# Kernel optimization log

Hardware: AMD Instinct MI355X
Metric: run time of the kernel (lower is better)

## Reference

```python
import jax, jax.numpy as jnp
import numpy as np

N_ENTITY = 100000
N_RELATION = 32
DIM = 64
N_LAYER = 2
B = 4096
T = 64


def setup_inputs() -> dict:
    key = jax.random.key(0)
    ks = jax.random.split(key, 12)
    inp = {
        "items": jax.random.randint(ks[0], (B,), 0, N_ENTITY),
        "user_h": jax.random.randint(ks[1], (N_LAYER, B, T), 0, N_ENTITY),
        "user_r": jax.random.randint(ks[2], (N_LAYER, B, T), 0, N_RELATION),
        "user_t": jax.random.randint(ks[3], (N_LAYER, B, T), 0, N_ENTITY),
        "item_h": jax.random.randint(ks[4], (N_LAYER, B, T), 0, N_ENTITY),
        "item_r": jax.random.randint(ks[5], (N_LAYER, B, T), 0, N_RELATION),
        "item_t": jax.random.randint(ks[6], (N_LAYER, B, T), 0, N_ENTITY),
        # parameters (xavier-ish scale)
        "entity_emb": jax.random.normal(ks[7], (N_ENTITY, DIM), jnp.float32) * 0.05,
        "relation_emb": jax.random.normal(ks[8], (N_RELATION, DIM), jnp.float32) * 0.05,
        # torch Linear(in,out,bias=False) stored here as [in, out] so y = x @ W
        "W1": jax.random.normal(ks[9], (2 * DIM, DIM), jnp.float32) * 0.1,
        "W2": jax.random.normal(ks[10], (DIM, DIM), jnp.float32) * 0.1,
        "W3": jax.random.normal(ks[11], (DIM, 1), jnp.float32) * 0.1,
    }
    return inp


def reference(items, user_h, user_r, user_t, item_h, item_r, item_t,
              entity_emb, relation_emb, W1, W2, W3):
    def knowledge_attention(h_idx, r_idx, t_idx):
        h = entity_emb[h_idx]        # [B, T, d]
        r = relation_emb[r_idx]      # [B, T, d]
        t = entity_emb[t_idx]        # [B, T, d]
        x = jnp.concatenate([h, r], axis=-1)           # [B, T, 2d]
        a = jax.nn.relu(x @ W1)                        # [B, T, d]
        a = jax.nn.relu(a @ W2)                        # [B, T, d]
        a = jax.nn.sigmoid(jnp.squeeze(a @ W3, -1))    # [B, T]
        w = jax.nn.softmax(a, axis=-1)                 # softmax over triples
        return jnp.sum(w[..., None] * t, axis=1)       # [B, d]

    # user embeddings: origin = mean of hop-0 heads, then attention per layer; agg='sum'
    e_u = jnp.mean(entity_emb[user_h[0]], axis=1)
    for i in range(N_LAYER):
        e_u = e_u + knowledge_attention(user_h[i], user_r[i], user_t[i])

    # item embeddings: origin = item entity emb, attention per layer,
    # plus (agg=='sum', n_layer>0) extra mean of hop-0 heads
    e_v = entity_emb[items]
    for i in range(N_LAYER):
        e_v = e_v + knowledge_attention(item_h[i], item_r[i], item_t[i])
    e_v = e_v + jnp.mean(entity_emb[item_h[0]], axis=1)

    scores = jax.nn.sigmoid(jnp.sum(e_v * e_u, axis=1))  # [B]
    return scores
```

## Files before the change

kernel.cpp:

```cpp
#include <hip/hip_runtime.h>
#include <hip/hip_bf16.h>
#include <cstdint>

#define DEV static __device__ __forceinline__

typedef float        v4f __attribute__((ext_vector_type(4)));
typedef float        v2f __attribute__((ext_vector_type(2)));
typedef short        v8s __attribute__((ext_vector_type(8)));
typedef unsigned int v4u __attribute__((ext_vector_type(4)));

static constexpr int N_ENT = 100000;
static constexpr int BATCH = 4096;

DEV unsigned short f2bf(float f) {
    __hip_bfloat16 h = __float2bfloat16(f);
    return __builtin_bit_cast(unsigned short, h);
}
DEV unsigned int pkbf(float lo, float hi) {
    return (unsigned)f2bf(lo) | ((unsigned)f2bf(hi) << 16);
}
DEV float bflo(unsigned int w) { return __uint_as_float(w << 16); }
DEV float bfhi(unsigned int w) { return __uint_as_float(w & 0xffff0000u); }
DEV v2f up2(unsigned int w) { return (v2f){bflo(w), bfhi(w)}; }

DEV void glds16(const void* g, void* l) {
    __builtin_amdgcn_global_load_lds(
        (const __attribute__((address_space(1))) unsigned int*)g,
        (__attribute__((address_space(3))) unsigned int*)l, 16, 0, 0);
}

__global__ void k0_prep(const float* __restrict__ rel, const float* __restrict__ W1,
                        const float* __restrict__ W2,
                        unsigned short* __restrict__ R1b, unsigned short* __restrict__ W2p,
                        unsigned short* __restrict__ W1p)
{
    const int gid = blockIdx.x * 256 + threadIdx.x;
    if (gid < 2048) {
        const int r = gid >> 6, j = gid & 63;
        float acc = 0.f;
        #pragma unroll 8
        for (int k = 0; k < 64; ++k)
            acc += rel[r * 64 + k] * W1[(64 + k) * 64 + j];
        R1b[gid] = f2bf(acc);
    } else if (gid < 2048 + 4096) {
        const int f = gid - 2048;
        const int i = f & 7, l = (f >> 3) & 63;
        const int tn = (f >> 9) & 3, kk = f >> 11;
        W2p[f] = f2bf(W2[(32 * kk + 8 * (l >> 4) + i) * 64 + 16 * tn + (l & 15)]);
    } else if (gid < 2048 + 8192) {
        const int f = gid - 6144;
        const int i = f & 7, l = (f >> 3) & 63;
        const int tn = (f >> 9) & 3, kk = f >> 11;
        W1p[f] = f2bf(W1[(32 * kk + 8 * (l >> 4) + i) * 64 + 16 * tn + (l & 15)]);
    }
}

__global__ void __launch_bounds__(256) k1_e1(const float* __restrict__ emb,
                                             const unsigned short* __restrict__ W1p,
                                             unsigned short* __restrict__ E1,
                                             unsigned short* __restrict__ E0)
{
    const int lane = threadIdx.x & 63;
    const int q = lane & 15, g = lane >> 4;
    const int wid = blockIdx.x * 4 + (threadIdx.x >> 6);
    const int e0 = wid * 16;
    if (e0 >= N_ENT) return;

    v8s af[2];
    #pragma unroll
    for (int kk = 0; kk < 2; ++kk) {
        const float* p = emb + (size_t)(e0 + q) * 64 + 32 * kk + 8 * g;
        const v4f x = *(const v4f*)p;
        const v4f y = *(const v4f*)(p + 4);
        v4u pk;
        pk[0] = pkbf(x[0], x[1]); pk[1] = pkbf(x[2], x[3]);
        pk[2] = pkbf(y[0], y[1]); pk[3] = pkbf(y[2], y[3]);
        af[kk] = __builtin_bit_cast(v8s, pk);
        *(v4u*)(E0 + (size_t)(e0 + q) * 64 + 32 * kk + 8 * g) = pk;
    }

    v4f acc[4];
    #pragma unroll
    for (int tn = 0; tn < 4; ++tn) acc[tn] = (v4f){0.f, 0.f, 0.f, 0.f};
    #pragma unroll
    for (int kk = 0; kk < 2; ++kk)
        #pragma unroll
        for (int tn = 0; tn < 4; ++tn) {
            const v8s bfr = *(const v8s*)(W1p + ((kk * 4 + tn) * 64 + lane) * 8);
            acc[tn] = __builtin_amdgcn_mfma_f32_16x16x32_bf16(af[kk], bfr, acc[tn], 0, 0, 0);
        }
    #pragma unroll
    for (int tn = 0; tn < 4; ++tn)
        #pragma unroll
        for (int i = 0; i < 4; ++i)
            E1[(size_t)(e0 + 4 * g + i) * 64 + 16 * tn + q] = f2bf(acc[tn][i]);
}

__global__ void __launch_bounds__(256) k2_fused(
    const int* __restrict__ items,
    const int* __restrict__ user_h, const int* __restrict__ user_r, const int* __restrict__ user_t,
    const int* __restrict__ item_h, const int* __restrict__ item_r, const int* __restrict__ item_t,
    const float* __restrict__ emb, const unsigned short* __restrict__ E0,
    const unsigned short* __restrict__ E1,
    const unsigned short* __restrict__ R1b, const unsigned short* __restrict__ W2p,
    const float* __restrict__ W3, float* __restrict__ out)
{
    __shared__ float ws_w[4][64];
    __shared__ float att_s[4][64];
    __shared__ float mp[4][64];
    __shared__ __align__(16) unsigned char e0s[4][8192];
    __shared__ __align__(16) unsigned char m0s[4][4096];

    const int lane  = threadIdx.x & 63;
    const int b     = blockIdx.x;
    const int combo = threadIdx.x >> 6;
    const int layer = combo & 1;
    const int side  = combo >> 1, half = combo & 1;
    const int* Hp; const int* Rp; const int* Tp;
    if (combo < 2) { Hp = user_h; Rp = user_r; Tp = user_t; }
    else           { Hp = item_h; Rp = item_r; Tp = item_t; }
    const int base = (layer * BATCH + b) * 64;
    const int* H0p = (side ? item_h : user_h) + b * 64;

    const int q = lane & 15, g = lane >> 4;
    const int sub = lane & 7, grp = lane >> 3;

    int hidx[4], ridx[4];
    #pragma unroll
    for (int tm = 0; tm < 4; ++tm) {
        hidx[tm] = Hp[base + 16 * tm + q];
        ridx[tm] = Rp[base + 16 * tm + q];
    }
    const int tv = Tp[base + lane];
    int midx[4];
    #pragma unroll
    for (int it = 0; it < 4; ++it) midx[it] = H0p[32 * half + 8 * it + grp];

    v4u ev[4][2], rv[4][2];
    #pragma unroll
    for (int tm = 0; tm < 4; ++tm)
        #pragma unroll
        for (int kk = 0; kk < 2; ++kk) {
            ev[tm][kk] = *(const v4u*)(E1  + (size_t)hidx[tm] * 64 + 32 * kk + 8 * g);
            rv[tm][kk] = *(const v4u*)(R1b + (size_t)ridx[tm] * 64 + 32 * kk + 8 * g);
        }

    #pragma unroll
    for (int it = 0; it < 8; ++it) {
        const int tr = __shfl(tv, 8 * it + grp);
        glds16(E0 + (size_t)tr * 64 + sub * 8, &e0s[combo][it * 1024]);
    }
    #pragma unroll
    for (int it = 0; it < 4; ++it)
        glds16(E0 + (size_t)midx[it] * 64 + sub * 8, &m0s[combo][it * 1024]);
    __builtin_amdgcn_sched_barrier(0);

    float w3v[4];
    #pragma unroll
    for (int tn = 0; tn < 4; ++tn) w3v[tn] = W3[16 * tn + q];

    float p[4][4];
    #pragma unroll
    for (int tm = 0; tm < 4; ++tm) {
        v4f a4[4];
        #pragma unroll
        for (int tn = 0; tn < 4; ++tn) a4[tn] = (v4f){0.f, 0.f, 0.f, 0.f};
        #pragma unroll
        for (int kk = 0; kk < 2; ++kk) {
            v4u afu;
            #pragma unroll
            for (int w = 0; w < 4; ++w) {
                const unsigned int e = ev[tm][kk][w], r = rv[tm][kk][w];
                afu[w] = pkbf(fmaxf(bflo(e) + bflo(r), 0.f),
                              fmaxf(bfhi(e) + bfhi(r), 0.f));
            }
            const v8s af = __builtin_bit_cast(v8s, afu);
            #pragma unroll
            for (int tn = 0; tn < 4; ++tn) {
                const v8s bfr = *(const v8s*)(W2p + ((kk * 4 + tn) * 64 + lane) * 8);
                a4[tn] = __builtin_amdgcn_mfma_f32_16x16x32_bf16(af, bfr, a4[tn], 0, 0, 0);
            }
        }
        #pragma unroll
        for (int i = 0; i < 4; ++i) {
            float s = 0.f;
            #pragma unroll
            for (int tn = 0; tn < 4; ++tn)
                s += fmaxf(a4[tn][i], 0.f) * w3v[tn];
            p[tm][i] = s;
        }
    }
    #pragma unroll
    for (int m = 1; m <= 8; m <<= 1)
        #pragma unroll
        for (int tm = 0; tm < 4; ++tm)
            #pragma unroll
            for (int i = 0; i < 4; ++i)
                p[tm][i] += __shfl_xor(p[tm][i], m);

    float ee[4][4];
    float sloc = 0.f;
    #pragma unroll
    for (int tm = 0; tm < 4; ++tm)
        #pragma unroll
        for (int i = 0; i < 4; ++i) {
            const float sg = 1.f / (1.f + __expf(-p[tm][i]));
            const float ex = __expf(sg);
            ee[tm][i] = ex;
            sloc += ex;
        }
    sloc += __shfl_xor(sloc, 16);
    sloc += __shfl_xor(sloc, 32);
    const float rS = 1.f / sloc;

    if (q == 0) {
        #pragma unroll
        for (int tm = 0; tm < 4; ++tm) {
            v4f wv;
            #pragma unroll
            for (int i = 0; i < 4; ++i) wv[i] = ee[tm][i] * rS;
            *(v4f*)&ws_w[combo][16 * tm + 4 * g] = wv;
        }
    }

    asm volatile("s_waitcnt vmcnt(0)" ::: "memory");
    __builtin_amdgcn_sched_barrier(0);

    v2f a2[4], m2[4];
    #pragma unroll
    for (int c = 0; c < 4; ++c) { a2[c] = (v2f){0.f, 0.f}; m2[c] = (v2f){0.f, 0.f}; }
    #pragma unroll
    for (int it = 0; it < 8; ++it) {
        const float w = ws_w[combo][8 * it + grp];
        const v2f wv = (v2f){w, w};
        const v4u e = *(const v4u*)&e0s[combo][it * 1024 + lane * 16];
        #pragma unroll
        for (int c = 0; c < 4; ++c) a2[c] += wv * up2(e[c]);
    }
    #pragma unroll
    for (int it = 0; it < 4; ++it) {
        const v4u e = *(const v4u*)&m0s[combo][it * 1024 + lane * 16];
        #pragma unroll
        for (int c = 0; c < 4; ++c) m2[c] += up2(e[c]);
    }
    #pragma unroll
    for (int m = 8; m <= 32; m <<= 1)
        #pragma unroll
        for (int c = 0; c < 4; ++c) {
            a2[c][0] += __shfl_xor(a2[c][0], m);
            a2[c][1] += __shfl_xor(a2[c][1], m);
            m2[c][0] += __shfl_xor(m2[c][0], m);
            m2[c][1] += __shfl_xor(m2[c][1], m);
        }
    if (lane < 8) {
        #pragma unroll
        for (int c = 0; c < 4; ++c) {
            att_s[combo][lane * 8 + 2 * c]     = a2[c][0];
            att_s[combo][lane * 8 + 2 * c + 1] = a2[c][1];
            mp[combo][lane * 8 + 2 * c]        = m2[c][0];
            mp[combo][lane * 8 + 2 * c + 1]    = m2[c][1];
        }
    }
    __syncthreads();

    if (threadIdx.x < 64) {
        const int j = lane;
        const float itemv = emb[(size_t)items[b] * 64 + j];
        const float eu = att_s[0][j] + att_s[1][j] + (mp[0][j] + mp[1][j]) * (1.f / 64.f);
        const float evv = itemv + att_s[2][j] + att_s[3][j]
                        + (mp[2][j] + mp[3][j]) * (1.f / 64.f);
        float d = eu * evv;
        #pragma unroll
        for (int m = 1; m <= 32; m <<= 1) d += __shfl_xor(d, m);
        if (lane == 0) out[b] = 1.f / (1.f + __expf(-d));
    }
}

extern "C" void kernel_launch(void* const* d_in, const int* in_sizes, int n_in,
                              void* d_out, int out_size, void* d_ws, size_t ws_size,
                              hipStream_t stream)
{
    const int*   items  = (const int*)d_in[0];
    const int*   user_h = (const int*)d_in[1];
    const int*   user_r = (const int*)d_in[2];
    const int*   user_t = (const int*)d_in[3];
    const int*   item_h = (const int*)d_in[4];
    const int*   item_r = (const int*)d_in[5];
    const int*   item_t = (const int*)d_in[6];
    const float* emb    = (const float*)d_in[7];
    const float* rel    = (const float*)d_in[8];
    const float* W1     = (const float*)d_in[9];
    const float* W2     = (const float*)d_in[10];
    const float* W3     = (const float*)d_in[11];
    float* out = (float*)d_out;

    char* ws = (char*)d_ws;
    const size_t tb = (size_t)N_ENT * 64 * 2;
    unsigned short* E0  = (unsigned short*)ws;
    unsigned short* E1  = (unsigned short*)(ws + tb);
    unsigned short* R1b = (unsigned short*)(ws + 2 * tb);
    unsigned short* W2p = (unsigned short*)(ws + 2 * tb + 4096);
    unsigned short* W1p = (unsigned short*)(ws + 2 * tb + 4096 + 8192);

    hipLaunchKernelGGL(k0_prep, dim3(40), dim3(256), 0, stream, rel, W1, W2, R1b, W2p, W1p);
    hipLaunchKernelGGL(k1_e1, dim3((6250 + 3) / 4), dim3(256), 0, stream, emb, W1p, E1, E0);
    hipLaunchKernelGGL(k2_fused, dim3(BATCH), dim3(256), 0, stream,
                       items, user_h, user_r, user_t, item_h, item_r, item_t,
                       emb, E0, E1, R1b, W2p, W3, out);
}
```

Measured before the change: 79.28 us.

## Split each attention combo across two waves with 512-thread blocks

The fused kernel now runs 8 waves per block instead of 4. Each (side, layer) combo is split across two waves that each handle 32 of the 64 triples. Softmax normalization moves to the end: each wave writes its partial denominator to shared memory and the final reduction divides by the combined sums. W2 fragments are preloaded into registers, and index loads are coalesced and redistributed with shuffles. The aim is more memory-level parallelism and shorter per-wave latency chains, at the cost of more waves per block and extra shared-memory bookkeeping.

```diff
diff --git a/kernel.cpp b/kernel.cpp
--- a/kernel.cpp
+++ b/kernel.cpp
@@ -96,7 +96,7 @@
             E1[(size_t)(e0 + 4 * g + i) * 64 + 16 * tn + q] = f2bf(acc[tn][i]);
 }
 
-__global__ void __launch_bounds__(256) k2_fused(
+__global__ void __launch_bounds__(512) k2_fused(
     const int* __restrict__ items,
     const int* __restrict__ user_h, const int* __restrict__ user_r, const int* __restrict__ user_t,
     const int* __restrict__ item_h, const int* __restrict__ item_r, const int* __restrict__ item_t,
@@ -106,62 +106,75 @@
     const float* __restrict__ W3, float* __restrict__ out)
 {
     __shared__ float ws_w[4][64];
-    __shared__ float att_s[4][64];
-    __shared__ float mp[4][64];
-    __shared__ __align__(16) unsigned char e0s[4][8192];
-    __shared__ __align__(16) unsigned char m0s[4][4096];
+    __shared__ float att_s[8][64];
+    __shared__ float mp[8][64];
+    __shared__ float sden[8];
+    __shared__ __align__(16) unsigned char e0s[8][4096];
+    __shared__ __align__(16) unsigned char m0s[8][2048];
 
     const int lane  = threadIdx.x & 63;
+    const int w     = threadIdx.x >> 6;
+    const int combo = w >> 1;
+    const int hs    = w & 1;
+    const int layer = combo & 1;
     const int b     = blockIdx.x;
-    const int combo = threadIdx.x >> 6;
-    const int layer = combo & 1;
-    const int side  = combo >> 1, half = combo & 1;
+
     const int* Hp; const int* Rp; const int* Tp;
     if (combo < 2) { Hp = user_h; Rp = user_r; Tp = user_t; }
     else           { Hp = item_h; Rp = item_r; Tp = item_t; }
     const int base = (layer * BATCH + b) * 64;
-    const int* H0p = (side ? item_h : user_h) + b * 64;
+    const int* mH = (w >= 4 ? item_h : user_h) + b * 64;
 
     const int q = lane & 15, g = lane >> 4;
     const int sub = lane & 7, grp = lane >> 3;
 
-    int hidx[4], ridx[4];
-    #pragma unroll
-    for (int tm = 0; tm < 4; ++tm) {
-        hidx[tm] = Hp[base + 16 * tm + q];
-        ridx[tm] = Rp[base + 16 * tm + q];
-    }
-    const int tv = Tp[base + lane];
-    int midx[4];
-    #pragma unroll
-    for (int it = 0; it < 4; ++it) midx[it] = H0p[32 * half + 8 * it + grp];
-
-    v4u ev[4][2], rv[4][2];
-    #pragma unroll
-    for (int tm = 0; tm < 4; ++tm)
+    const int hv  = Hp[base + lane];
+    const int rv_ = Rp[base + lane];
+    const int tvv = Tp[base + lane];
+    const int mhv = mH[lane];
+    float w3v[4];
+    #pragma unroll
+    for (int tn = 0; tn < 4; ++tn) w3v[tn] = W3[16 * tn + q];
+
+    int hidx[2], ridx[2];
+    #pragma unroll
+    for (int tmi = 0; tmi < 2; ++tmi) {
+        hidx[tmi] = __shfl(hv,  16 * (2 * hs + tmi) + q);
+        ridx[tmi] = __shfl(rv_, 16 * (2 * hs + tmi) + q);
+    }
+
+    v4u ev[2][2], rvv[2][2];
+    #pragma unroll
+    for (int tmi = 0; tmi < 2; ++tmi)
         #pragma unroll
         for (int kk = 0; kk < 2; ++kk) {
-            ev[tm][kk] = *(const v4u*)(E1  + (size_t)hidx[tm] * 64 + 32 * kk + 8 * g);
-            rv[tm][kk] = *(const v4u*)(R1b + (size_t)ridx[tm] * 64 + 32 * kk + 8 * g);
-        }
-
-    #pragma unroll
-    for (int it = 0; it < 8; ++it) {
-        const int tr = __shfl(tv, 8 * it + grp);
-        glds16(E0 + (size_t)tr * 64 + sub * 8, &e0s[combo][it * 1024]);
-    }
-    #pragma unroll
-    for (int it = 0; it < 4; ++it)
-        glds16(E0 + (size_t)midx[it] * 64 + sub * 8, &m0s[combo][it * 1024]);
+            ev[tmi][kk]  = *(const v4u*)(E1  + (size_t)hidx[tmi] * 64 + 32 * kk + 8 * g);
+            rvv[tmi][kk] = *(const v4u*)(R1b + (size_t)ridx[tmi] * 64 + 32 * kk + 8 * g);
+        }
+
+    v8s bfr[2][4];
+    #pragma unroll
+    for (int kk = 0; kk < 2; ++kk)
+        #pragma unroll
+        for (int tn = 0; tn < 4; ++tn)
+            bfr[kk][tn] = *(const v8s*)(W2p + ((kk * 4 + tn) * 64 + lane) * 8);
+
     __builtin_amdgcn_sched_barrier(0);
-
-    float w3v[4];
-    #pragma unroll
-    for (int tn = 0; tn < 4; ++tn) w3v[tn] = W3[16 * tn + q];
-
-    float p[4][4];
-    #pragma unroll
-    for (int tm = 0; tm < 4; ++tm) {
+    #pragma unroll
+    for (int it = 0; it < 4; ++it) {
+        const int tr = __shfl(tvv, 32 * hs + 8 * it + grp);
+        glds16(E0 + (size_t)tr * 64 + sub * 8, &e0s[w][it * 1024]);
+    }
+    #pragma unroll
+    for (int it = 0; it < 2; ++it) {
+        const int mi = __shfl(mhv, 16 * (w & 3) + 8 * it + grp);
+        glds16(E0 + (size_t)mi * 64 + sub * 8, &m0s[w][it * 1024]);
+    }
+    __builtin_amdgcn_sched_barrier(0);
+
+    float p[2][4];
+    #pragma unroll
+    for (int tmi = 0; tmi < 2; ++tmi) {
         v4f a4[4];
         #pragma unroll
         for (int tn = 0; tn < 4; ++tn) a4[tn] = (v4f){0.f, 0.f, 0.f, 0.f};
@@ -169,17 +182,15 @@
         for (int kk = 0; kk < 2; ++kk) {
             v4u afu;
             #pragma unroll
-            for (int w = 0; w < 4; ++w) {
-                const unsigned int e = ev[tm][kk][w], r = rv[tm][kk][w];
-                afu[w] = pkbf(fmaxf(bflo(e) + bflo(r), 0.f),
+            for (int x = 0; x < 4; ++x) {
+                const unsigned int e = ev[tmi][kk][x], r = rvv[tmi][kk][x];
+                afu[x] = pkbf(fmaxf(bflo(e) + bflo(r), 0.f),
                               fmaxf(bfhi(e) + bfhi(r), 0.f));
             }
             const v8s af = __builtin_bit_cast(v8s, afu);
             #pragma unroll
-            for (int tn = 0; tn < 4; ++tn) {
-                const v8s bfr = *(const v8s*)(W2p + ((kk * 4 + tn) * 64 + lane) * 8);
-                a4[tn] = __builtin_amdgcn_mfma_f32_16x16x32_bf16(af, bfr, a4[tn], 0, 0, 0);
-            }
+            for (int tn = 0; tn < 4; ++tn)
+                a4[tn] = __builtin_amdgcn_mfma_f32_16x16x32_bf16(af, bfr[kk][tn], a4[tn], 0, 0, 0);
         }
         #pragma unroll
         for (int i = 0; i < 4; ++i) {
@@ -187,39 +198,39 @@
             #pragma unroll
             for (int tn = 0; tn < 4; ++tn)
                 s += fmaxf(a4[tn][i], 0.f) * w3v[tn];
-            p[tm][i] = s;
+            p[tmi][i] = s;
         }
     }
     #pragma unroll
     for (int m = 1; m <= 8; m <<= 1)
         #pragma unroll
-        for (int tm = 0; tm < 4; ++tm)
+        for (int tmi = 0; tmi < 2; ++tmi)
             #pragma unroll
             for (int i = 0; i < 4; ++i)
-                p[tm][i] += __shfl_xor(p[tm][i], m);
-
-    float ee[4][4];
+                p[tmi][i] += __shfl_xor(p[tmi][i], m);
+
+    float ee[2][4];
     float sloc = 0.f;
     #pragma unroll
-    for (int tm = 0; tm < 4; ++tm)
+    for (int tmi = 0; tmi < 2; ++tmi)
         #pragma unroll
         for (int i = 0; i < 4; ++i) {
-            const float sg = 1.f / (1.f + __expf(-p[tm][i]));
+            const float sg = 1.f / (1.f + __expf(-p[tmi][i]));
             const float ex = __expf(sg);
-            ee[tm][i] = ex;
+            ee[tmi][i] = ex;
             sloc += ex;
         }
     sloc += __shfl_xor(sloc, 16);
     sloc += __shfl_xor(sloc, 32);
-    const float rS = 1.f / sloc;
+    if (lane == 0) sden[w] = sloc;
 
     if (q == 0) {
         #pragma unroll
-        for (int tm = 0; tm < 4; ++tm) {
+        for (int tmi = 0; tmi < 2; ++tmi) {
             v4f wv;
             #pragma unroll
-            for (int i = 0; i < 4; ++i) wv[i] = ee[tm][i] * rS;
-            *(v4f*)&ws_w[combo][16 * tm + 4 * g] = wv;
+            for (int i = 0; i < 4; ++i) wv[i] = ee[tmi][i];
+            *(v4f*)&ws_w[combo][16 * (2 * hs + tmi) + 4 * g] = wv;
         }
     }
 
@@ -230,16 +241,16 @@
     #pragma unroll
     for (int c = 0; c < 4; ++c) { a2[c] = (v2f){0.f, 0.f}; m2[c] = (v2f){0.f, 0.f}; }
     #pragma unroll
-    for (int it = 0; it < 8; ++it) {
-        const float w = ws_w[combo][8 * it + grp];
-        const v2f wv = (v2f){w, w};
-        const v4u e = *(const v4u*)&e0s[combo][it * 1024 + lane * 16];
+    for (int it = 0; it < 4; ++it) {
+        const float wgt = ws_w[combo][32 * hs + 8 * it + grp];
+        const v2f wv = (v2f){wgt, wgt};
+        const v4u e = *(const v4u*)&e0s[w][it * 1024 + lane * 16];
         #pragma unroll
         for (int c = 0; c < 4; ++c) a2[c] += wv * up2(e[c]);
     }
     #pragma unroll
-    for (int it = 0; it < 4; ++it) {
-        const v4u e = *(const v4u*)&m0s[combo][it * 1024 + lane * 16];
+    for (int it = 0; it < 2; ++it) {
+        const v4u e = *(const v4u*)&m0s[w][it * 1024 + lane * 16];
         #pragma unroll
         for (int c = 0; c < 4; ++c) m2[c] += up2(e[c]);
     }
@@ -255,20 +266,30 @@
     if (lane < 8) {
         #pragma unroll
         for (int c = 0; c < 4; ++c) {
-            att_s[combo][lane * 8 + 2 * c]     = a2[c][0];
-            att_s[combo][lane * 8 + 2 * c + 1] = a2[c][1];
-            mp[combo][lane * 8 + 2 * c]        = m2[c][0];
-            mp[combo][lane * 8 + 2 * c + 1]    = m2[c][1];
-        }
-    }
+            att_s[w][lane * 8 + 2 * c]     = a2[c][0];
+            att_s[w][lane * 8 + 2 * c + 1] = a2[c][1];
+            mp[w][lane * 8 + 2 * c]        = m2[c][0];
+            mp[w][lane * 8 + 2 * c + 1]    = m2[c][1];
+        }
+    }
+
+    float itemv = 0.f;
+    if (w == 0) itemv = emb[(size_t)items[b] * 64 + lane];
     __syncthreads();
 
-    if (threadIdx.x < 64) {
+    if (w == 0) {
+        const float rS0 = 1.f / (sden[0] + sden[1]);
+        const float rS1 = 1.f / (sden[2] + sden[3]);
+        const float rS2 = 1.f / (sden[4] + sden[5]);
+        const float rS3 = 1.f / (sden[6] + sden[7]);
         const int j = lane;
-        const float itemv = emb[(size_t)items[b] * 64 + j];
-        const float eu = att_s[0][j] + att_s[1][j] + (mp[0][j] + mp[1][j]) * (1.f / 64.f);
-        const float evv = itemv + att_s[2][j] + att_s[3][j]
-                        + (mp[2][j] + mp[3][j]) * (1.f / 64.f);
+        const float eu = (att_s[0][j] + att_s[1][j]) * rS0
+                       + (att_s[2][j] + att_s[3][j]) * rS1
+                       + (mp[0][j] + mp[1][j] + mp[2][j] + mp[3][j]) * (1.f / 64.f);
+        const float evv = itemv
+                       + (att_s[4][j] + att_s[5][j]) * rS2
+                       + (att_s[6][j] + att_s[7][j]) * rS3
+                       + (mp[4][j] + mp[5][j] + mp[6][j] + mp[7][j]) * (1.f / 64.f);
         float d = eu * evv;
         #pragma unroll
         for (int m = 1; m <= 32; m <<= 1) d += __shfl_xor(d, m);
@@ -304,7 +325,7 @@
 
     hipLaunchKernelGGL(k0_prep, dim3(40), dim3(256), 0, stream, rel, W1, W2, R1b, W2p, W1p);
     hipLaunchKernelGGL(k1_e1, dim3((6250 + 3) / 4), dim3(256), 0, stream, emb, W1p, E1, E0);
-    hipLaunchKernelGGL(k2_fused, dim3(BATCH), dim3(256), 0, stream,
+    hipLaunchKernelGGL(k2_fused, dim3(BATCH), dim3(512), 0, stream,
                        items, user_h, user_r, user_t, item_h, item_r, item_t,
                        emb, E0, E1, R1b, W2p, W3, out);
 }
```

New measurement: 85.21 us. 1.07x slower.

## Store projected entity table E1 and relation table in FP8, stage relations in LDS

Applied to the files above, without the earlier changes.

The precomputed entity-times-W1 table E1 and the relation projection R1 are now stored as FP8 (e4m3) instead of bf16. This halves the bytes of the gathered E1 rows and the table written by k1. k1's MFMA operands are swapped so each lane writes contiguous packed FP8 words. In k2, the small relation table is staged into LDS once per block, and W2 fragments are hoisted into registers. The cost is lower precision in the first-layer pre-activation, which could hurt accuracy against the reference tolerance.

```diff
diff --git a/kernel.cpp b/kernel.cpp
--- a/kernel.cpp
+++ b/kernel.cpp
@@ -8,6 +8,7 @@
 typedef float        v2f __attribute__((ext_vector_type(2)));
 typedef short        v8s __attribute__((ext_vector_type(8)));
 typedef unsigned int v4u __attribute__((ext_vector_type(4)));
+typedef unsigned int v2u __attribute__((ext_vector_type(2)));
 
 static constexpr int N_ENT = 100000;
 static constexpr int BATCH = 4096;
@@ -22,6 +23,13 @@
 DEV float bflo(unsigned int w) { return __uint_as_float(w << 16); }
 DEV float bfhi(unsigned int w) { return __uint_as_float(w & 0xffff0000u); }
 DEV v2f up2(unsigned int w) { return (v2f){bflo(w), bfhi(w)}; }
+
+template <bool HI> DEV v2f dec8(unsigned int u) {
+    return __builtin_amdgcn_cvt_pk_f32_fp8((int)u, HI);
+}
+template <bool HI> DEV unsigned int enc8(float a, float b, unsigned int old) {
+    return __builtin_amdgcn_cvt_pk_fp8_f32(a, b, (int)old, HI);
+}
 
 DEV void glds16(const void* g, void* l) {
     __builtin_amdgcn_global_load_lds(
@@ -31,24 +39,28 @@
 
 __global__ void k0_prep(const float* __restrict__ rel, const float* __restrict__ W1,
                         const float* __restrict__ W2,
-                        unsigned short* __restrict__ R1b, unsigned short* __restrict__ W2p,
+                        unsigned char* __restrict__ R1f, unsigned short* __restrict__ W2p,
                         unsigned short* __restrict__ W1p)
 {
     const int gid = blockIdx.x * 256 + threadIdx.x;
-    if (gid < 2048) {
-        const int r = gid >> 6, j = gid & 63;
-        float acc = 0.f;
+    if (gid < 1024) {
+        const int r = gid >> 5, jp = gid & 31;
+        float d0 = 0.f, d1 = 0.f;
         #pragma unroll 8
-        for (int k = 0; k < 64; ++k)
-            acc += rel[r * 64 + k] * W1[(64 + k) * 64 + j];
-        R1b[gid] = f2bf(acc);
-    } else if (gid < 2048 + 4096) {
-        const int f = gid - 2048;
+        for (int k = 0; k < 64; ++k) {
+            const float rv = rel[r * 64 + k];
+            d0 += rv * W1[(64 + k) * 64 + 2 * jp];
+            d1 += rv * W1[(64 + k) * 64 + 2 * jp + 1];
+        }
+        const unsigned int u = enc8<false>(d0, d1, 0u);
+        ((unsigned short*)R1f)[r * 32 + jp] = (unsigned short)(u & 0xffffu);
+    } else if (gid < 1024 + 4096) {
+        const int f = gid - 1024;
         const int i = f & 7, l = (f >> 3) & 63;
         const int tn = (f >> 9) & 3, kk = f >> 11;
         W2p[f] = f2bf(W2[(32 * kk + 8 * (l >> 4) + i) * 64 + 16 * tn + (l & 15)]);
-    } else if (gid < 2048 + 8192) {
-        const int f = gid - 6144;
+    } else if (gid < 1024 + 8192) {
+        const int f = gid - 5120;
         const int i = f & 7, l = (f >> 3) & 63;
         const int tn = (f >> 9) & 3, kk = f >> 11;
         W1p[f] = f2bf(W1[(32 * kk + 8 * (l >> 4) + i) * 64 + 16 * tn + (l & 15)]);
@@ -57,7 +69,7 @@
 
 __global__ void __launch_bounds__(256) k1_e1(const float* __restrict__ emb,
                                              const unsigned short* __restrict__ W1p,
-                                             unsigned short* __restrict__ E1,
+                                             unsigned char* __restrict__ E1f,
                                              unsigned short* __restrict__ E0)
 {
     const int lane = threadIdx.x & 63;
@@ -66,7 +78,7 @@
     const int e0 = wid * 16;
     if (e0 >= N_ENT) return;
 
-    v8s af[2];
+    v8s bf[2];
     #pragma unroll
     for (int kk = 0; kk < 2; ++kk) {
         const float* p = emb + (size_t)(e0 + q) * 64 + 32 * kk + 8 * g;
@@ -75,25 +87,26 @@
         v4u pk;
         pk[0] = pkbf(x[0], x[1]); pk[1] = pkbf(x[2], x[3]);
         pk[2] = pkbf(y[0], y[1]); pk[3] = pkbf(y[2], y[3]);
-        af[kk] = __builtin_bit_cast(v8s, pk);
+        bf[kk] = __builtin_bit_cast(v8s, pk);
         *(v4u*)(E0 + (size_t)(e0 + q) * 64 + 32 * kk + 8 * g) = pk;
     }
 
     v4f acc[4];
     #pragma unroll
-    for (int tn = 0; tn < 4; ++tn) acc[tn] = (v4f){0.f, 0.f, 0.f, 0.f};
+    for (int tile = 0; tile < 4; ++tile) acc[tile] = (v4f){0.f, 0.f, 0.f, 0.f};
     #pragma unroll
     for (int kk = 0; kk < 2; ++kk)
         #pragma unroll
-        for (int tn = 0; tn < 4; ++tn) {
-            const v8s bfr = *(const v8s*)(W1p + ((kk * 4 + tn) * 64 + lane) * 8);
-            acc[tn] = __builtin_amdgcn_mfma_f32_16x16x32_bf16(af[kk], bfr, acc[tn], 0, 0, 0);
-        }
-    #pragma unroll
-    for (int tn = 0; tn < 4; ++tn)
-        #pragma unroll
-        for (int i = 0; i < 4; ++i)
-            E1[(size_t)(e0 + 4 * g + i) * 64 + 16 * tn + q] = f2bf(acc[tn][i]);
+        for (int tile = 0; tile < 4; ++tile) {
+            const v8s w1f = *(const v8s*)(W1p + ((kk * 4 + tile) * 64 + lane) * 8);
+            acc[tile] = __builtin_amdgcn_mfma_f32_16x16x32_bf16(w1f, bf[kk], acc[tile], 0, 0, 0);
+        }
+    #pragma unroll
+    for (int tile = 0; tile < 4; ++tile) {
+        unsigned int u = enc8<false>(acc[tile][0], acc[tile][1], 0u);
+        u = enc8<true>(acc[tile][2], acc[tile][3], u);
+        *(unsigned int*)(E1f + (size_t)(e0 + q) * 64 + 16 * tile + 4 * g) = u;
+    }
 }
 
 __global__ void __launch_bounds__(256) k2_fused(
@@ -101,13 +114,14 @@
     const int* __restrict__ user_h, const int* __restrict__ user_r, const int* __restrict__ user_t,
     const int* __restrict__ item_h, const int* __restrict__ item_r, const int* __restrict__ item_t,
     const float* __restrict__ emb, const unsigned short* __restrict__ E0,
-    const unsigned short* __restrict__ E1,
-    const unsigned short* __restrict__ R1b, const unsigned short* __restrict__ W2p,
+    const unsigned char* __restrict__ E1f,
+    const unsigned char* __restrict__ R1f, const unsigned short* __restrict__ W2p,
     const float* __restrict__ W3, float* __restrict__ out)
 {
     __shared__ float ws_w[4][64];
     __shared__ float att_s[4][64];
     __shared__ float mp[4][64];
+    __shared__ __align__(16) unsigned char r1s[2048];
     __shared__ __align__(16) unsigned char e0s[4][8192];
     __shared__ __align__(16) unsigned char m0s[4][4096];
 
@@ -135,15 +149,28 @@
     int midx[4];
     #pragma unroll
     for (int it = 0; it < 4; ++it) midx[it] = H0p[32 * half + 8 * it + grp];
-
-    v4u ev[4][2], rv[4][2];
+    float w3v[4];
+    #pragma unroll
+    for (int tn = 0; tn < 4; ++tn) w3v[tn] = W3[16 * tn + q];
+    v8s bfr[2][4];
+    #pragma unroll
+    for (int kk = 0; kk < 2; ++kk)
+        #pragma unroll
+        for (int tn = 0; tn < 4; ++tn)
+            bfr[kk][tn] = *(const v8s*)(W2p + ((kk * 4 + tn) * 64 + lane) * 8);
+
+    if (threadIdx.x < 128) {
+        const v4u t = *(const v4u*)(R1f + threadIdx.x * 16);
+        *(v4u*)&r1s[threadIdx.x * 16] = t;
+    }
+    __syncthreads();
+
+    v2u ev[4][2];
     #pragma unroll
     for (int tm = 0; tm < 4; ++tm)
         #pragma unroll
-        for (int kk = 0; kk < 2; ++kk) {
-            ev[tm][kk] = *(const v4u*)(E1  + (size_t)hidx[tm] * 64 + 32 * kk + 8 * g);
-            rv[tm][kk] = *(const v4u*)(R1b + (size_t)ridx[tm] * 64 + 32 * kk + 8 * g);
-        }
+        for (int kk = 0; kk < 2; ++kk)
+            ev[tm][kk] = *(const v2u*)(E1f + (size_t)hidx[tm] * 64 + 32 * kk + 8 * g);
 
     #pragma unroll
     for (int it = 0; it < 8; ++it) {
@@ -155,9 +182,12 @@
         glds16(E0 + (size_t)midx[it] * 64 + sub * 8, &m0s[combo][it * 1024]);
     __builtin_amdgcn_sched_barrier(0);
 
-    float w3v[4];
-    #pragma unroll
-    for (int tn = 0; tn < 4; ++tn) w3v[tn] = W3[16 * tn + q];
+    v2u rv[4][2];
+    #pragma unroll
+    for (int tm = 0; tm < 4; ++tm)
+        #pragma unroll
+        for (int kk = 0; kk < 2; ++kk)
+            rv[tm][kk] = *(const v2u*)&r1s[ridx[tm] * 64 + 32 * kk + 8 * g];
 
     float p[4][4];
     #pragma unroll
@@ -167,19 +197,20 @@
         for (int tn = 0; tn < 4; ++tn) a4[tn] = (v4f){0.f, 0.f, 0.f, 0.f};
         #pragma unroll
         for (int kk = 0; kk < 2; ++kk) {
+            const v2u e8 = ev[tm][kk], r8 = rv[tm][kk];
+            v2f a01 = dec8<false>(e8[0]) + dec8<false>(r8[0]);
+            v2f a23 = dec8<true>(e8[0])  + dec8<true>(r8[0]);
+            v2f a45 = dec8<false>(e8[1]) + dec8<false>(r8[1]);
+            v2f a67 = dec8<true>(e8[1])  + dec8<true>(r8[1]);
             v4u afu;
-            #pragma unroll
-            for (int w = 0; w < 4; ++w) {
-                const unsigned int e = ev[tm][kk][w], r = rv[tm][kk][w];
-                afu[w] = pkbf(fmaxf(bflo(e) + bflo(r), 0.f),
-                              fmaxf(bfhi(e) + bfhi(r), 0.f));
-            }
+            afu[0] = pkbf(fmaxf(a01[0], 0.f), fmaxf(a01[1], 0.f));
+            afu[1] = pkbf(fmaxf(a23[0], 0.f), fmaxf(a23[1], 0.f));
+            afu[2] = pkbf(fmaxf(a45[0], 0.f), fmaxf(a45[1], 0.f));
+            afu[3] = pkbf(fmaxf(a67[0], 0.f), fmaxf(a67[1], 0.f));
             const v8s af = __builtin_bit_cast(v8s, afu);
             #pragma unroll
-            for (int tn = 0; tn < 4; ++tn) {
-                const v8s bfr = *(const v8s*)(W2p + ((kk * 4 + tn) * 64 + lane) * 8);
-                a4[tn] = __builtin_amdgcn_mfma_f32_16x16x32_bf16(af, bfr, a4[tn], 0, 0, 0);
-            }
+            for (int tn = 0; tn < 4; ++tn)
+                a4[tn] = __builtin_amdgcn_mfma_f32_16x16x32_bf16(af, bfr[kk][tn], a4[tn], 0, 0, 0);
         }
         #pragma unroll
         for (int i = 0; i < 4; ++i) {
@@ -295,16 +326,17 @@
     float* out = (float*)d_out;
 
     char* ws = (char*)d_ws;
-    const size_t tb = (size_t)N_ENT * 64 * 2;
+    const size_t e0b = (size_t)N_ENT * 64 * 2;
+    const size_t e1b = (size_t)N_ENT * 64;
     unsigned short* E0  = (unsigned short*)ws;
-    unsigned short* E1  = (unsigned short*)(ws + tb);
-    unsigned short* R1b = (unsigned short*)(ws + 2 * tb);
-    unsigned short* W2p = (unsigned short*)(ws + 2 * tb + 4096);
-    unsigned short* W1p = (unsigned short*)(ws + 2 * tb + 4096 + 8192);
-
-    hipLaunchKernelGGL(k0_prep, dim3(40), dim3(256), 0, stream, rel, W1, W2, R1b, W2p, W1p);
-    hipLaunchKernelGGL(k1_e1, dim3((6250 + 3) / 4), dim3(256), 0, stream, emb, W1p, E1, E0);
+    unsigned char*  E1f = (unsigned char*)(ws + e0b);
+    unsigned char*  R1f = (unsigned char*)(ws + e0b + e1b);
+    unsigned short* W2p = (unsigned short*)(ws + e0b + e1b + 2048);
+    unsigned short* W1p = (unsigned short*)(ws + e0b + e1b + 2048 + 8192);
+
+    hipLaunchKernelGGL(k0_prep, dim3(36), dim3(256), 0, stream, rel, W1, W2, R1f, W2p, W1p);
+    hipLaunchKernelGGL(k1_e1, dim3((6250 + 3) / 4), dim3(256), 0, stream, emb, W1p, E1f, E0);
     hipLaunchKernelGGL(k2_fused, dim3(BATCH), dim3(256), 0, stream,
                        items, user_h, user_r, user_t, item_h, item_r, item_t,
-                       emb, E0, E1, R1b, W2p, W3, out);
-}
+                       emb, E0, E1f, R1f, W2p, W3, out);
+}
```

After: 91.71 us. 15.7% more time.
